# Kernel tuning notes

Hardware: AMD Instinct MI355X
Metric: run time of the kernel (lower is better)

Reference implementation:

```python
import jax, jax.numpy as jnp
import numpy as np

N_NODES = 50000
N_EDGES = 800000
F_IN = 128
HID = 32
HEADS = 8
NEG_SLOPE = 0.2  # PyG GATConv default leaky_relu slope


def gat_conv(x, src, dst, W, a_src, a_dst, b, num_nodes):
    """PyG-style GATConv (eval mode, self-loops already included in src/dst).
    W: [F_in, H*C], a_src/a_dst: [H, C], b: [H*C]."""
    H, C = a_src.shape
    h = (x @ W).reshape(num_nodes, H, C)                      # [N,H,C]
    alpha_s = jnp.einsum('nhc,hc->nh', h, a_src)              # [N,H]
    alpha_d = jnp.einsum('nhc,hc->nh', h, a_dst)
    e = jax.nn.leaky_relu(alpha_s[src] + alpha_d[dst], NEG_SLOPE)  # [E,H]
    # numerically-stable softmax over edges grouped by destination node
    m = jax.ops.segment_max(e, dst, num_segments=num_nodes)  # [N,H]
    e = jnp.exp(e - m[dst])
    denom = jax.ops.segment_sum(e, dst, num_segments=num_nodes)
    alpha = e / denom[dst]                                    # [E,H]
    msg = h[src] * alpha[:, :, None]                          # [E,H,C]
    out = jax.ops.segment_sum(msg, dst, num_segments=num_nodes)  # [N,H,C]
    return out.reshape(num_nodes, H * C) + b


def setup_inputs() -> dict:
    key = jax.random.key(0)
    ks = jax.random.split(key, 10)
    x = jax.random.normal(ks[0], (N_NODES, F_IN), dtype=jnp.float32)
    edge_index = jax.random.randint(ks[1], (2, N_EDGES), 0, N_NODES, dtype=jnp.int64)
    s = 0.1
    W1 = jax.random.normal(ks[2], (F_IN, HEADS * HID), dtype=jnp.float32) * s
    att_src1 = jax.random.normal(ks[3], (HEADS, HID), dtype=jnp.float32) * s
    att_dst1 = jax.random.normal(ks[4], (HEADS, HID), dtype=jnp.float32) * s
    b1 = jnp.zeros((HEADS * HID,), dtype=jnp.float32)
    W2 = jax.random.normal(ks[5], (HEADS * HID, HID), dtype=jnp.float32) * s
    att_src2 = jax.random.normal(ks[6], (1, HID), dtype=jnp.float32) * s
    att_dst2 = jax.random.normal(ks[7], (1, HID), dtype=jnp.float32) * s
    b2 = jnp.zeros((HID,), dtype=jnp.float32)
    return {"x": x, "edge_index": edge_index, "W1": W1, "att_src1": att_src1,
            "att_dst1": att_dst1, "b1": b1, "W2": W2, "att_src2": att_src2,
            "att_dst2": att_dst2, "b2": b2}


def reference(x, edge_index, W1, att_src1, att_dst1, b1, W2, att_src2, att_dst2, b2):
    num_nodes = x.shape[0]
    # PyG GATConv adds self-loops by default
    loop = jnp.arange(num_nodes, dtype=edge_index.dtype)
    src = jnp.concatenate([edge_index[0], loop])
    dst = jnp.concatenate([edge_index[1], loop])
    h = gat_conv(x, src, dst, W1, att_src1, att_dst1, b1, num_nodes)  # [N, 8*HID]
    h = jax.nn.elu(h)
    # dropout is identity in eval mode
    out = gat_conv(h, src, dst, W2, att_src2, att_dst2, b2, num_nodes)  # [N, HID]
    return out
```

## Files before the change

kernel.cpp:

```cpp
#include <hip/hip_runtime.h>

#define F_IN 128
#define HC1 256
#define HID 32
#define HEADS 8
#define MAXDEG 64

#define BW    256
#define NB    196
#define NR    8
#define RCAP  768
#define BCAP  64
#define CHUNK 4096

typedef _Float16 h16;
typedef h16 f16x2 __attribute__((ext_vector_type(2)));
typedef h16 f16x4 __attribute__((ext_vector_type(4)));
typedef h16 f16x8 __attribute__((ext_vector_type(8)));
typedef float f32x4 __attribute__((ext_vector_type(4)));

union U2 { unsigned u; f16x2 h; };
union U4 { uint2 u; f16x4 h4; f16x2 h2[2]; };
union U8 { uint4 u; f16x8 h8; f16x2 h2[4]; };

__device__ __forceinline__ unsigned pkexp(float t){
  t = fminf(fmaxf(t, -30.f), 5.f);
  U2 r; r.h = (f16x2){ (h16)__expf(t), (h16)__expf(0.2f*t) };
  return r.u;
}

__global__ void k_prep(const float* __restrict__ w1, const float* __restrict__ w2,
                       const float* __restrict__ as1w, const float* __restrict__ ad1w,
                       h16* __restrict__ w1t, h16* __restrict__ w2t,
                       h16* __restrict__ awt, int* __restrict__ gcur){
  int t = blockIdx.x*blockDim.x + threadIdx.x;
  if (t < NB*NR) gcur[t] = 0;
  if (t < HC1*F_IN){
    int n = t >> 7, k = t & 127;
    w1t[t] = (h16)w1[(size_t)k*HC1 + n];
  } else if (t < HC1*F_IN + HID*HC1){
    int u = t - HC1*F_IN;
    int n = u >> 8, k = u & 255;
    w2t[u] = (h16)w2[(size_t)k*HID + n];
  } else if (t < HC1*F_IN + HID*HC1 + 16*F_IN){
    int u = t - HC1*F_IN - HID*HC1;
    int c = u >> 7, k = u & 127;
    int h = c & 7;
    const float* a = (c < 8) ? as1w : ad1w;
    float s = 0.f;
    #pragma unroll
    for (int j = 0; j < 32; ++j) s += w1[(size_t)k*HC1 + h*HID + j] * a[h*HID + j];
    awt[u] = (h16)s;
  }
}

__global__ __launch_bounds__(256) void k_bin(const int* __restrict__ srcA,
    const int* __restrict__ dstA, int* __restrict__ gcur,
    uint2* __restrict__ rec, int E){
  __shared__ int   cl[NB];
  __shared__ int   bl[NB];
  __shared__ uint2 buf[NB][BCAP];
  int tid = threadIdx.x;
  for (int t = tid; t < NB; t += 256) cl[t] = 0;
  __syncthreads();
  int e0 = blockIdx.x*CHUNK;
  #pragma unroll
  for (int j = 0; j < CHUNK; j += 256){
    int e = e0 + j + tid;
    if (e < E){
      int d = dstA[e], s = srcA[e];
      int b = d >> 8;
      int p = atomicAdd(&cl[b], 1);
      if (p < BCAP) buf[b][p] = make_uint2((unsigned)d, (unsigned)s);
    }
  }
  __syncthreads();
  int r = blockIdx.x & (NR-1);
  if (tid < NB){
    int c = cl[tid]; if (c > BCAP) c = BCAP;
    cl[tid] = c;
    bl[tid] = (c > 0) ? atomicAdd(&gcur[tid*NR + r], c) : 0;
  }
  __syncthreads();
  int wv = tid >> 6, lane = tid & 63;
  for (int b = wv; b < NB; b += 4){
    int c = cl[b];
    if (lane < c){
      int idx = bl[b] + lane;
      if (idx < RCAP) rec[(size_t)(b*NR + r)*RCAP + idx] = buf[b][lane];
    }
  }
}

__global__ __launch_bounds__(256) void k_csr(const uint2* __restrict__ rec,
    const int* __restrict__ gcur, int* __restrict__ cnt, int* __restrict__ csr, int N){
  __shared__ int cl[BW];
  int tid = threadIdx.x;
  int b = blockIdx.x;
  if (tid < BW) cl[tid] = 0;
  __syncthreads();
  for (int r = 0; r < NR; ++r){
    int len = gcur[b*NR + r]; if (len > RCAP) len = RCAP;
    const uint2* rr = rec + (size_t)(b*NR + r)*RCAP;
    for (int i = tid; i < len; i += 256){
      uint2 v = rr[i];
      int d = (int)v.x, s = (int)v.y;
      int slot = atomicAdd(&cl[d & (BW-1)], 1);
      if (slot < MAXDEG) csr[d*MAXDEG + slot] = s;
    }
  }
  __syncthreads();
  int d = b*BW + tid;
  if (tid < BW && d < N) cnt[d] = cl[tid];
}

__global__ __launch_bounds__(256) void k_gemm1(const float* __restrict__ x,
    const h16* __restrict__ w1t, const h16* __restrict__ awt,
    h16* __restrict__ h1h,
    unsigned* __restrict__ es1p, unsigned* __restrict__ ed1p, int M){
  int tid = threadIdx.x;
  __shared__ h16 As[64][136];
  __shared__ h16 Bs[64][136];
  __shared__ h16 Aw[16][136];
  int rowbase = blockIdx.x * 64;
  #pragma unroll
  for (int j = 0; j < 8; ++j){
    int idx = (tid + 256*j) * 4;
    int r = idx >> 7, c = idx & 127;
    int row = rowbase + r;
    float4 v = make_float4(0.f,0.f,0.f,0.f);
    if (row < M) v = *(const float4*)(x + (size_t)row*F_IN + c);
    U4 q; q.h4 = (f16x4){ (h16)v.x, (h16)v.y, (h16)v.z, (h16)v.w };
    *(uint2*)&As[r][c] = q.u;
  }
  {
    int idx = tid * 8;
    int c = idx >> 7, k = idx & 127;
    *(uint4*)&Aw[c][k] = *(const uint4*)(awt + idx);
  }
  int wv = tid >> 6, lane = tid & 63;
  int lr = lane & 15, lq = lane >> 4;
  int mrow = wv*16 + lr;

  #pragma unroll
  for (int q = 0; q < 4; ++q){
    __syncthreads();
    #pragma unroll
    for (int j = 0; j < 4; ++j){
      int idx = (tid + 256*j) * 8;
      int r = idx >> 7, c = idx & 127;
      *(uint4*)&Bs[r][c] = *(const uint4*)(w1t + (size_t)(q*64 + r)*F_IN + c);
    }
    __syncthreads();
    f32x4 acc[4] = {};
    #pragma unroll
    for (int k0 = 0; k0 < F_IN; k0 += 32){
      f16x8 a = *(const f16x8*)&As[mrow][k0 + lq*8];
      #pragma unroll
      for (int cb = 0; cb < 4; ++cb){
        f16x8 b = *(const f16x8*)&Bs[cb*16 + lr][k0 + lq*8];
        acc[cb] = __builtin_amdgcn_mfma_f32_16x16x32_f16(a, b, acc[cb], 0, 0, 0);
      }
    }
    #pragma unroll
    for (int cb = 0; cb < 4; ++cb){
      #pragma unroll
      for (int r = 0; r < 4; ++r){
        int row = rowbase + wv*16 + lq*4 + r;
        int col = q*64 + cb*16 + lr;
        if (row < M) h1h[(size_t)row*HC1 + col] = (h16)acc[cb][r];
      }
    }
  }
  {
    f32x4 aacc = {};
    #pragma unroll
    for (int k0 = 0; k0 < F_IN; k0 += 32){
      f16x8 a = *(const f16x8*)&As[mrow][k0 + lq*8];
      f16x8 b = *(const f16x8*)&Aw[lr][k0 + lq*8];
      aacc = __builtin_amdgcn_mfma_f32_16x16x32_f16(a, b, aacc, 0, 0, 0);
    }
    int h = lr & 7;
    unsigned* dstp = (lr < 8) ? es1p : ed1p;
    #pragma unroll
    for (int r = 0; r < 4; ++r){
      int row = rowbase + wv*16 + lq*4 + r;
      if (row < M) dstp[row*HEADS + h] = pkexp(aacc[r]);
    }
  }
}

__global__ __launch_bounds__(256) void k_agg1(const h16* __restrict__ h1h,
    const unsigned* __restrict__ es1p, const unsigned* __restrict__ ed1p,
    const int* __restrict__ cnt, const int* __restrict__ csr,
    const float* __restrict__ b1,
    const h16* __restrict__ w2t, const float* __restrict__ as2w,
    const float* __restrict__ ad2w,
    h16* __restrict__ g2h, unsigned* __restrict__ es2p, unsigned* __restrict__ ed2p,
    int N){
  __shared__ h16 Ws2[32][264];
  __shared__ h16 h2s[4][256];
  int tid = threadIdx.x;
  #pragma unroll
  for (int j = 0; j < 4; ++j){
    int idx = (tid + 256*j) * 8;
    int n = idx >> 8, k = idx & 255;
    *(uint4*)&Ws2[n][k] = *(const uint4*)(w2t + idx);
  }
  int wv = tid >> 6, lane = tid & 63;
  int w0 = blockIdx.x*4 + wv;
  bool valid = w0 < N;
  int w = valid ? w0 : N-1;
  int c0 = lane << 2;
  int h = lane >> 3;
  U2 ed; ed.u = ed1p[w*HEADS + h];
  U2 es; es.u = es1p[w*HEADS + h];
  f16x2 pp = es.h * ed.h;
  h16 pm = pp[0] > pp[1] ? pp[0] : pp[1];
  f16x2 pv = { pm, pm };
  U4 sv; sv.u = *(const uint2*)(h1h + (size_t)w*HC1 + c0);
  f16x2 a01 = pv * sv.h2[0];
  f16x2 a23 = pv * sv.h2[1];
  float l = (float)pm;
  int i = w*MAXDEG;
  int d = cnt[w]; if (d > MAXDEG) d = MAXDEG;
  int e1 = i + d;
  for (; i + 4 <= e1; i += 4){
    int sA = csr[i], sB = csr[i+1], sC = csr[i+2], sD = csr[i+3];
    U2 eA, eB, eC, eD;
    eA.u = es1p[sA*HEADS + h]; eB.u = es1p[sB*HEADS + h];
    eC.u = es1p[sC*HEADS + h]; eD.u = es1p[sD*HEADS + h];
    U4 uA, uB, uC, uD;
    uA.u = *(const uint2*)(h1h + (size_t)sA*HC1 + c0);
    uB.u = *(const uint2*)(h1h + (size_t)sB*HC1 + c0);
    uC.u = *(const uint2*)(h1h + (size_t)sC*HC1 + c0);
    uD.u = *(const uint2*)(h1h + (size_t)sD*HC1 + c0);
    f16x2 pA2 = eA.h * ed.h, pB2 = eB.h * ed.h;
    f16x2 pC2 = eC.h * ed.h, pD2 = eD.h * ed.h;
    h16 pA = pA2[0] > pA2[1] ? pA2[0] : pA2[1];
    h16 pB = pB2[0] > pB2[1] ? pB2[0] : pB2[1];
    h16 pC = pC2[0] > pC2[1] ? pC2[0] : pC2[1];
    h16 pD = pD2[0] > pD2[1] ? pD2[0] : pD2[1];
    f16x2 vA = { pA, pA }, vB = { pB, pB }, vC = { pC, pC }, vD = { pD, pD };
    a01 += vA * uA.h2[0]; a23 += vA * uA.h2[1];
    a01 += vB * uB.h2[0]; a23 += vB * uB.h2[1];
    a01 += vC * uC.h2[0]; a23 += vC * uC.h2[1];
    a01 += vD * uD.h2[0]; a23 += vD * uD.h2[1];
    l += (float)pA + (float)pB + (float)pC + (float)pD;
  }
  for (; i < e1; ++i){
    int s = csr[i];
    U2 e; e.u = es1p[s*HEADS + h];
    U4 u; u.u = *(const uint2*)(h1h + (size_t)s*HC1 + c0);
    f16x2 p2 = e.h * ed.h;
    h16 p = p2[0] > p2[1] ? p2[0] : p2[1];
    f16x2 pv2 = { p, p };
    a01 += pv2 * u.h2[0]; a23 += pv2 * u.h2[1];
    l += (float)p;
  }
  float rl = 1.f / l;
  float4 bb = *(const float4*)(b1 + c0);
  float o0 = (float)a01[0]*rl + bb.x;
  float o1 = (float)a01[1]*rl + bb.y;
  float o2 = (float)a23[0]*rl + bb.z;
  float o3 = (float)a23[1]*rl + bb.w;
  o0 = o0 > 0.f ? o0 : __expf(o0) - 1.f;
  o1 = o1 > 0.f ? o1 : __expf(o1) - 1.f;
  o2 = o2 > 0.f ? o2 : __expf(o2) - 1.f;
  o3 = o3 > 0.f ? o3 : __expf(o3) - 1.f;
  U4 pk; pk.h4 = (f16x4){ (h16)o0, (h16)o1, (h16)o2, (h16)o3 };
  *(uint2*)&h2s[wv][c0] = pk.u;
  __syncthreads();

  int j = lane & 31, hs = lane >> 5;
  const h16* hrow = &h2s[wv][hs*128];
  const h16* wrow = &Ws2[j][hs*128];
  f16x2 acA = {0,0}, acB = {0,0};
  #pragma unroll
  for (int cb = 0; cb < 16; ++cb){
    U8 hv, wv8;
    hv.h8  = *(const f16x8*)(hrow + cb*8);
    wv8.h8 = *(const f16x8*)(wrow + cb*8);
    acA += hv.h2[0]*wv8.h2[0];
    acB += hv.h2[1]*wv8.h2[1];
    acA += hv.h2[2]*wv8.h2[2];
    acB += hv.h2[3]*wv8.h2[3];
  }
  f16x2 ac = acA + acB;
  float g = (float)ac[0] + (float)ac[1];
  g += __shfl_xor(g, 32, 64);
  if (valid && hs == 0) g2h[(size_t)w0*HID + j] = (h16)g;
  float ps = g * as2w[j];
  float pd = g * ad2w[j];
  #pragma unroll
  for (int mask = 1; mask <= 16; mask <<= 1){
    ps += __shfl_xor(ps, mask, 64);
    pd += __shfl_xor(pd, mask, 64);
  }
  if (valid && lane == 0){
    es2p[w0] = pkexp(ps);
    ed2p[w0] = pkexp(pd);
  }
}

__global__ __launch_bounds__(256) void k_agg2(const h16* __restrict__ g2h,
    const unsigned* __restrict__ es2p, const unsigned* __restrict__ ed2p,
    const int* __restrict__ cnt, const int* __restrict__ csr,
    const float* __restrict__ b2, float* __restrict__ out, int N){
  int tid = threadIdx.x;
  int w = blockIdx.x*8 + (tid >> 6)*2 + ((tid & 63) >> 5);
  if (w >= N) return;
  int l32 = tid & 31;
  int grp = l32 >> 3;
  int cl  = l32 & 7;
  int c0 = cl << 2;
  U2 ed; ed.u = ed2p[w];
  U4 acc; acc.h2[0] = (f16x2){0,0}; acc.h2[1] = (f16x2){0,0};
  float l = 0.f;
  if (grp == 0){
    U2 es; es.u = es2p[w];
    f16x2 pp = es.h * ed.h;
    h16 pm = pp[0] > pp[1] ? pp[0] : pp[1];
    f16x2 pv = { pm, pm };
    U4 u; u.u = *(const uint2*)(g2h + (size_t)w*HID + c0);
    acc.h2[0] = pv * u.h2[0]; acc.h2[1] = pv * u.h2[1];
    l = (float)pm;
  }
  int s0 = w*MAXDEG;
  int d = cnt[w]; if (d > MAXDEG) d = MAXDEG;
  int e1 = s0 + d;
  for (int i = s0 + grp; i < e1; i += 4){
    int s = csr[i];
    U2 es; es.u = es2p[s];
    U4 u; u.u = *(const uint2*)(g2h + (size_t)s*HID + c0);
    f16x2 pp = es.h * ed.h;
    h16 pm = pp[0] > pp[1] ? pp[0] : pp[1];
    f16x2 pv = { pm, pm };
    acc.h2[0] += pv * u.h2[0];
    acc.h2[1] += pv * u.h2[1];
    l += (float)pm;
  }
  #pragma unroll
  for (int mask = 8; mask <= 16; mask <<= 1){
    l += __shfl_xor(l, mask, 64);
    U4 o;
    o.u.x = __shfl_xor(acc.u.x, mask, 64);
    o.u.y = __shfl_xor(acc.u.y, mask, 64);
    acc.h2[0] += o.h2[0]; acc.h2[1] += o.h2[1];
  }
  if (grp == 0){
    float rl = 1.f / l;
    float4 bb = *(const float4*)(b2 + c0);
    *(float4*)(out + (size_t)w*HID + c0) = make_float4(
      (float)acc.h4[0]*rl + bb.x, (float)acc.h4[1]*rl + bb.y,
      (float)acc.h4[2]*rl + bb.z, (float)acc.h4[3]*rl + bb.w);
  }
}

extern "C" void kernel_launch(void* const* d_in, const int* in_sizes, int n_in,
                              void* d_out, int out_size, void* d_ws, size_t ws_size,
                              hipStream_t stream){
  const float* x    = (const float*)d_in[0];
  const int*   ei   = (const int*)d_in[1];
  const float* W1   = (const float*)d_in[2];
  const float* as1w = (const float*)d_in[3];
  const float* ad1w = (const float*)d_in[4];
  const float* b1   = (const float*)d_in[5];
  const float* W2   = (const float*)d_in[6];
  const float* as2w = (const float*)d_in[7];
  const float* ad2w = (const float*)d_in[8];
  const float* b2   = (const float*)d_in[9];
  float* out = (float*)d_out;

  const int N = in_sizes[0] / F_IN;
  const int E = in_sizes[1] / 2;
  const int* srcA = ei;
  const int* dstA = ei + E;

  unsigned* es1p = (unsigned*)d_ws;
  unsigned* ed1p = es1p + (size_t)N*HEADS;
  unsigned* es2p = ed1p + (size_t)N*HEADS;
  unsigned* ed2p = es2p + N;
  h16* w1t = (h16*)(ed2p + N);
  h16* w2t = w1t + (size_t)HC1*F_IN;
  h16* awt = w2t + (size_t)HID*HC1;
  h16* h1h = awt + (size_t)16*F_IN;
  h16* g2h = h1h + (size_t)N*HC1;
  int* cnt = (int*)(g2h + (size_t)N*HID);
  int* csr = cnt + N;

  uint2* rec = (uint2*)h1h;
  int* gcur  = (int*)g2h;

  int prepT = HC1*F_IN + HID*HC1 + 16*F_IN;
  int prepG = (N > prepT ? N : prepT);
  k_prep <<<(prepG+255)/256, 256, 0, stream>>>(W1, W2, as1w, ad1w, w1t, w2t, awt, gcur);

  int gb = (E + CHUNK - 1)/CHUNK;
  k_bin  <<<gb, 256, 0, stream>>>(srcA, dstA, gcur, rec, E);
  k_csr  <<<NB, 256, 0, stream>>>(rec, gcur, cnt, csr, N);

  int g1 = (N + 63)/64;
  k_gemm1 <<<g1, 256, 0, stream>>>(x, w1t, awt, h1h, es1p, ed1p, N);
  k_agg1  <<<(N + 3)/4, 256, 0, stream>>>(h1h, es1p, ed1p, cnt, csr, b1,
                                          w2t, as2w, ad2w, g2h, es2p, ed2p, N);
  k_agg2  <<<(N + 7)/8, 256, 0, stream>>>(g2h, es2p, ed2p, cnt, csr, b2, out, N);
}
```

Measured before the change: 225.9 us.

## Use head-major layout for layer-1 features and split aggregation by head

Layer-1 features and attention scores are now stored head-major, as [head][node][32] instead of [node][256]. The layer-1 aggregation is split so that each block handles a single head over 32 destination nodes, which narrows each head's gather to a 3.2MB slice so it fits in cache better. The layer-2 GEMV moves into its own kernel, so the ELU output h2 takes an extra global-memory round trip and one more kernel launch. CSR indices are read with nontemporal loads.

After: 323.5 us. 1.43x slower.

```diff
diff --git a/kernel.cpp b/kernel.cpp
--- a/kernel.cpp
+++ b/kernel.cpp
@@ -168,7 +168,8 @@
       for (int r = 0; r < 4; ++r){
         int row = rowbase + wv*16 + lq*4 + r;
         int col = q*64 + cb*16 + lr;
-        if (row < M) h1h[(size_t)row*HC1 + col] = (h16)acc[cb][r];
+        int hd = col >> 5, cc = col & 31;
+        if (row < M) h1h[((size_t)hd*M + row)*HID + cc] = (h16)acc[cb][r];
       }
     }
   }
@@ -185,56 +186,49 @@
     #pragma unroll
     for (int r = 0; r < 4; ++r){
       int row = rowbase + wv*16 + lq*4 + r;
-      if (row < M) dstp[row*HEADS + h] = pkexp(aacc[r]);
-    }
-  }
-}
-
-__global__ __launch_bounds__(256) void k_agg1(const h16* __restrict__ h1h,
+      if (row < M) dstp[(size_t)h*M + row] = pkexp(aacc[r]);
+    }
+  }
+}
+
+__global__ __launch_bounds__(256) void k_agg1h(const h16* __restrict__ h1h,
     const unsigned* __restrict__ es1p, const unsigned* __restrict__ ed1p,
     const int* __restrict__ cnt, const int* __restrict__ csr,
-    const float* __restrict__ b1,
-    const h16* __restrict__ w2t, const float* __restrict__ as2w,
-    const float* __restrict__ ad2w,
-    h16* __restrict__ g2h, unsigned* __restrict__ es2p, unsigned* __restrict__ ed2p,
-    int N){
-  __shared__ h16 Ws2[32][264];
-  __shared__ h16 h2s[4][256];
-  int tid = threadIdx.x;
-  #pragma unroll
-  for (int j = 0; j < 4; ++j){
-    int idx = (tid + 256*j) * 8;
-    int n = idx >> 8, k = idx & 255;
-    *(uint4*)&Ws2[n][k] = *(const uint4*)(w2t + idx);
-  }
+    const float* __restrict__ b1, h16* __restrict__ h2, int N){
+  int tid = threadIdx.x;
+  int head  = blockIdx.x & 7;
+  int chunk = blockIdx.x >> 3;
   int wv = tid >> 6, lane = tid & 63;
-  int w0 = blockIdx.x*4 + wv;
-  bool valid = w0 < N;
-  int w = valid ? w0 : N-1;
-  int c0 = lane << 2;
-  int h = lane >> 3;
-  U2 ed; ed.u = ed1p[w*HEADS + h];
-  U2 es; es.u = es1p[w*HEADS + h];
+  int grp = lane >> 3, cl = lane & 7;
+  int d = chunk*32 + wv*8 + grp;
+  if (d >= N) return;
+  size_t hb = (size_t)head * N;
+  const h16* hh = h1h + hb*HID;
+  U2 ed; ed.u = ed1p[hb + d];
+  U2 es; es.u = es1p[hb + d];
   f16x2 pp = es.h * ed.h;
   h16 pm = pp[0] > pp[1] ? pp[0] : pp[1];
   f16x2 pv = { pm, pm };
-  U4 sv; sv.u = *(const uint2*)(h1h + (size_t)w*HC1 + c0);
+  U4 sv; sv.u = *(const uint2*)(hh + (size_t)d*HID + cl*4);
   f16x2 a01 = pv * sv.h2[0];
   f16x2 a23 = pv * sv.h2[1];
   float l = (float)pm;
-  int i = w*MAXDEG;
-  int d = cnt[w]; if (d > MAXDEG) d = MAXDEG;
-  int e1 = i + d;
-  for (; i + 4 <= e1; i += 4){
-    int sA = csr[i], sB = csr[i+1], sC = csr[i+2], sD = csr[i+3];
+  int deg = cnt[d]; if (deg > MAXDEG) deg = MAXDEG;
+  const int* crow = csr + d*MAXDEG;
+  int i = 0;
+  for (; i + 4 <= deg; i += 4){
+    int sA = __builtin_nontemporal_load(crow + i);
+    int sB = __builtin_nontemporal_load(crow + i + 1);
+    int sC = __builtin_nontemporal_load(crow + i + 2);
+    int sD = __builtin_nontemporal_load(crow + i + 3);
     U2 eA, eB, eC, eD;
-    eA.u = es1p[sA*HEADS + h]; eB.u = es1p[sB*HEADS + h];
-    eC.u = es1p[sC*HEADS + h]; eD.u = es1p[sD*HEADS + h];
+    eA.u = es1p[hb + sA]; eB.u = es1p[hb + sB];
+    eC.u = es1p[hb + sC]; eD.u = es1p[hb + sD];
     U4 uA, uB, uC, uD;
-    uA.u = *(const uint2*)(h1h + (size_t)sA*HC1 + c0);
-    uB.u = *(const uint2*)(h1h + (size_t)sB*HC1 + c0);
-    uC.u = *(const uint2*)(h1h + (size_t)sC*HC1 + c0);
-    uD.u = *(const uint2*)(h1h + (size_t)sD*HC1 + c0);
+    uA.u = *(const uint2*)(hh + (size_t)sA*HID + cl*4);
+    uB.u = *(const uint2*)(hh + (size_t)sB*HID + cl*4);
+    uC.u = *(const uint2*)(hh + (size_t)sC*HID + cl*4);
+    uD.u = *(const uint2*)(hh + (size_t)sD*HID + cl*4);
     f16x2 pA2 = eA.h * ed.h, pB2 = eB.h * ed.h;
     f16x2 pC2 = eC.h * ed.h, pD2 = eD.h * ed.h;
     h16 pA = pA2[0] > pA2[1] ? pA2[0] : pA2[1];
@@ -248,18 +242,18 @@
     a01 += vD * uD.h2[0]; a23 += vD * uD.h2[1];
     l += (float)pA + (float)pB + (float)pC + (float)pD;
   }
-  for (; i < e1; ++i){
-    int s = csr[i];
-    U2 e; e.u = es1p[s*HEADS + h];
-    U4 u; u.u = *(const uint2*)(h1h + (size_t)s*HC1 + c0);
+  for (; i < deg; ++i){
+    int s = __builtin_nontemporal_load(crow + i);
+    U2 e; e.u = es1p[hb + s];
+    U4 u; u.u = *(const uint2*)(hh + (size_t)s*HID + cl*4);
     f16x2 p2 = e.h * ed.h;
     h16 p = p2[0] > p2[1] ? p2[0] : p2[1];
-    f16x2 pv2 = { p, p };
-    a01 += pv2 * u.h2[0]; a23 += pv2 * u.h2[1];
+    f16x2 pw = { p, p };
+    a01 += pw * u.h2[0]; a23 += pw * u.h2[1];
     l += (float)p;
   }
   float rl = 1.f / l;
-  float4 bb = *(const float4*)(b1 + c0);
+  float4 bb = *(const float4*)(b1 + head*HID + cl*4);
   float o0 = (float)a01[0]*rl + bb.x;
   float o1 = (float)a01[1]*rl + bb.y;
   float o2 = (float)a23[0]*rl + bb.z;
@@ -269,7 +263,28 @@
   o2 = o2 > 0.f ? o2 : __expf(o2) - 1.f;
   o3 = o3 > 0.f ? o3 : __expf(o3) - 1.f;
   U4 pk; pk.h4 = (f16x4){ (h16)o0, (h16)o1, (h16)o2, (h16)o3 };
-  *(uint2*)&h2s[wv][c0] = pk.u;
+  *(uint2*)&h2[(size_t)d*HC1 + head*HID + cl*4] = pk.u;
+}
+
+__global__ __launch_bounds__(256) void k_gemv(const h16* __restrict__ h2,
+    const h16* __restrict__ w2t, const float* __restrict__ as2w,
+    const float* __restrict__ ad2w,
+    h16* __restrict__ g2h, unsigned* __restrict__ es2p, unsigned* __restrict__ ed2p,
+    int N){
+  __shared__ h16 Ws2[32][264];
+  __shared__ h16 h2s[4][256];
+  int tid = threadIdx.x;
+  #pragma unroll
+  for (int j = 0; j < 4; ++j){
+    int idx = (tid + 256*j) * 8;
+    int n = idx >> 8, k = idx & 255;
+    *(uint4*)&Ws2[n][k] = *(const uint4*)(w2t + idx);
+  }
+  int wv = tid >> 6, lane = tid & 63;
+  int w0 = blockIdx.x*4 + wv;
+  bool valid = w0 < N;
+  int w = valid ? w0 : N-1;
+  *(uint2*)&h2s[wv][lane*4] = *(const uint2*)(h2 + (size_t)w*HC1 + lane*4);
   __syncthreads();
 
   int j = lane & 31, hs = lane >> 5;
@@ -388,6 +403,7 @@
   h16* g2h = h1h + (size_t)N*HC1;
   int* cnt = (int*)(g2h + (size_t)N*HID);
   int* csr = cnt + N;
+  h16* h2  = (h16*)(csr + (size_t)N*MAXDEG);
 
   uint2* rec = (uint2*)h1h;
   int* gcur  = (int*)g2h;
@@ -402,7 +418,9 @@
 
   int g1 = (N + 63)/64;
   k_gemm1 <<<g1, 256, 0, stream>>>(x, w1t, awt, h1h, es1p, ed1p, N);
-  k_agg1  <<<(N + 3)/4, 256, 0, stream>>>(h1h, es1p, ed1p, cnt, csr, b1,
-                                          w2t, as2w, ad2w, g2h, es2p, ed2p, N);
+
+  int chunks = (N + 31)/32;
+  k_agg1h <<<chunks*8, 256, 0, stream>>>(h1h, es1p, ed1p, cnt, csr, b1, h2, N);
+  k_gemv  <<<(N + 3)/4, 256, 0, stream>>>(h2, w2t, as2w, ad2w, g2h, es2p, ed2p, N);
   k_agg2  <<<(N + 7)/8, 256, 0, stream>>>(g2h, es2p, ed2p, cnt, csr, b2, out, N);
 }
```
